# Kernel optimization log

Hardware: AMD Instinct MI355X
Metric: run time of the kernel (lower is better)

The kernel has to match this reference:

```python
import jax, jax.numpy as jnp
import numpy as np

DIM = 4096
BATCH = 8192
NUM_LAYERS = 6
STRENGTHS = (0.1, 0.1, 0.05)  # entail, contra, neutral
EPS_NORM = 1e-12  # torch F.normalize eps
MAX_NORM = 10.0


def _normalize(x, axis=-1):
    n = jnp.linalg.norm(x, axis=axis, keepdims=True)
    return x / jnp.maximum(n, EPS_NORM)


def setup_inputs() -> dict:
    key = jax.random.key(0)
    k0, k1, k2, k3 = jax.random.split(key, 4)
    return {
        "h0": jax.random.normal(k0, (BATCH, DIM), dtype=jnp.float32),
        "anchor_entail": jax.random.normal(k1, (DIM,), dtype=jnp.float32),
        "anchor_contra": jax.random.normal(k2, (DIM,), dtype=jnp.float32),
        "anchor_neutral": jax.random.normal(k3, (DIM,), dtype=jnp.float32),
    }


def reference(h0, anchor_entail, anchor_contra, anchor_neutral):
    # Normalized fixed anchor directions, stacked [3, dim] (E, C, N)
    dirs = jnp.stack([
        _normalize(anchor_entail, axis=0),
        _normalize(anchor_contra, axis=0),
        _normalize(anchor_neutral, axis=0),
    ])  # [3, dim]
    strengths = jnp.asarray(STRENGTHS, dtype=h0.dtype)  # [3]

    def step(h, _):
        h_n = _normalize(h)                         # [B, dim]
        align = jnp.einsum("bd,kd->bk", h_n, dirs)  # [B, 3]
        div = 1.0 - align                           # divergence_from_alignment
        tens = jnp.maximum(div, 0.0)                # tension (clamp min=0)
        # normalized direction away from each anchor: [B, 3, dim]
        vec = _normalize(h[:, None, :] - dirs[None, :, :])
        force = jnp.einsum("bk,bkd->bd", strengths[None, :] * div, vec)
        h = h - force
        h_norm = jnp.linalg.norm(h, axis=-1, keepdims=True)
        h = jnp.where(h_norm > MAX_NORM, h * (MAX_NORM / (h_norm + 1e-8)), h)
        return h, (align, div, tens)

    h_final, (aligns, divs, tensions) = jax.lax.scan(step, h0, None, length=NUM_LAYERS)
    # traces: [num_layers, B, 3] with anchor order (entail, contra, neutral)
    return h_final, aligns, divs, tensions
```

## Files before the change

kernel.cpp:

```cpp
#include <hip/hip_runtime.h>


constexpr int DIM = 4096;
constexpr int BATCH = 8192;
constexpr int NLAYERS = 6;
constexpr int TPB = 256;
constexpr int VPT = DIM / (TPB * 4);

constexpr size_t HOUT = (size_t)BATCH * DIM;
constexpr size_t TRACE = (size_t)NLAYERS * BATCH * 3;
constexpr size_t OFF_ALIGN = HOUT;
constexpr size_t OFF_DIV   = HOUT + TRACE;
constexpr size_t OFF_TENS  = HOUT + 2 * TRACE;

__device__ __forceinline__ float wave_red(float v) {
#pragma unroll
  for (int off = 32; off > 0; off >>= 1) v += __shfl_down(v, off, 64);
  return v;
}

__global__ __launch_bounds__(TPB) void gram_kernel(
    const float* __restrict__ an0, const float* __restrict__ an1,
    const float* __restrict__ an2, float* __restrict__ ws) {
  const int tid = threadIdx.x;
  float r[6];
#pragma unroll
  for (int i = 0; i < 6; ++i) r[i] = 0.f;
#pragma unroll
  for (int j = 0; j < VPT; ++j) {
    const int idx = (tid + j * TPB) * 4;
    const float4 x = *(const float4*)(an0 + idx);
    const float4 y = *(const float4*)(an1 + idx);
    const float4 z = *(const float4*)(an2 + idx);
    r[0] += x.x*x.x + x.y*x.y + x.z*x.z + x.w*x.w;
    r[1] += y.x*y.x + y.y*y.y + y.z*y.z + y.w*y.w;
    r[2] += z.x*z.x + z.y*z.y + z.z*z.z + z.w*z.w;
    r[3] += x.x*y.x + x.y*y.y + x.z*y.z + x.w*y.w;
    r[4] += x.x*z.x + x.y*z.y + x.z*z.z + x.w*z.w;
    r[5] += y.x*z.x + y.y*z.y + y.z*z.z + y.w*z.w;
  }
  __shared__ float lds[4][6];
  const int lane = tid & 63, wv = tid >> 6;
#pragma unroll
  for (int i = 0; i < 6; ++i) r[i] = wave_red(r[i]);
  if (lane == 0) {
#pragma unroll
    for (int i = 0; i < 6; ++i) lds[wv][i] = r[i];
  }
  __syncthreads();
  if (tid == 0) {
#pragma unroll
    for (int i = 0; i < 6; ++i)
      r[i] = lds[0][i] + lds[1][i] + lds[2][i] + lds[3][i];
    const float n0 = fmaxf(sqrtf(r[0]), 1e-12f);
    const float n1 = fmaxf(sqrtf(r[1]), 1e-12f);
    const float n2 = fmaxf(sqrtf(r[2]), 1e-12f);
    ws[0] = n0; ws[1] = n1; ws[2] = n2;
    ws[3] = r[3] / (n0 * n1);
    ws[4] = r[4] / (n0 * n2);
    ws[5] = r[5] / (n1 * n2);
    ws[6] = r[0] / (n0 * n0);
    ws[7] = r[1] / (n1 * n1);
    ws[8] = r[2] / (n2 * n2);
  }
}

__global__ __launch_bounds__(TPB) void collapse_kernel(
    const float* __restrict__ h0,
    const float* __restrict__ an0,
    const float* __restrict__ an1,
    const float* __restrict__ an2,
    const float* __restrict__ ws,
    float* __restrict__ out) {
  const int b = blockIdx.x;
  const int tid = threadIdx.x;
  const float* hrow = h0 + (size_t)b * DIM;

  float4 hv[VPT];
  float r[4] = {0.f, 0.f, 0.f, 0.f};
#pragma unroll
  for (int j = 0; j < VPT; ++j) {
    const int idx = (tid + j * TPB) * 4;
    hv[j] = *(const float4*)(hrow + idx);
    const float4 x = *(const float4*)(an0 + idx);
    const float4 y = *(const float4*)(an1 + idx);
    const float4 z = *(const float4*)(an2 + idx);
    const float4 h = hv[j];
    r[0] += h.x*h.x + h.y*h.y + h.z*h.z + h.w*h.w;
    r[1] += h.x*x.x + h.y*x.y + h.z*x.z + h.w*x.w;
    r[2] += h.x*y.x + h.y*y.y + h.z*y.z + h.w*y.w;
    r[3] += h.x*z.x + h.y*z.y + h.z*z.z + h.w*z.w;
  }

  __shared__ float lds[4][4];
  __shared__ float coef[4];
  const int lane = tid & 63, wv = tid >> 6;
#pragma unroll
  for (int i = 0; i < 4; ++i) r[i] = wave_red(r[i]);
  if (lane == 0) {
#pragma unroll
    for (int i = 0; i < 4; ++i) lds[wv][i] = r[i];
  }
  __syncthreads();

  if (tid == 0) {
#pragma unroll
    for (int i = 0; i < 4; ++i)
      r[i] = lds[0][i] + lds[1][i] + lds[2][i] + lds[3][i];
    const float n0 = ws[0], n1 = ws[1], n2 = ws[2];
    float G[3][3];
    G[0][1] = G[1][0] = ws[3];
    G[0][2] = G[2][0] = ws[4];
    G[1][2] = G[2][1] = ws[5];
    G[0][0] = ws[6]; G[1][1] = ws[7]; G[2][2] = ws[8];

    const float str[3] = {0.1f, 0.1f, 0.05f};
    float s = r[0];
    float d[3] = {r[1] / n0, r[2] / n1, r[3] / n2};
    float A = 1.f;
    float B[3] = {0.f, 0.f, 0.f};

#pragma unroll
    for (int l = 0; l < NLAYERS; ++l) {
      const float hn = fmaxf(sqrtf(s), 1e-12f);
      float al[3], dv[3], c[3];
#pragma unroll
      for (int k = 0; k < 3; ++k) {
        al[k] = d[k] / hn;
        dv[k] = 1.f - al[k];
        const float rr = fmaxf(sqrtf(s - 2.f * d[k] + G[k][k]), 1e-12f);
        c[k] = str[k] * dv[k] / rr;
      }
#pragma unroll
      for (int k = 0; k < 3; ++k) {
        const size_t o = (size_t)l * (BATCH * 3) + (size_t)b * 3 + k;
        out[OFF_ALIGN + o] = al[k];
        out[OFF_DIV + o]   = dv[k];
        out[OFF_TENS + o]  = fmaxf(dv[k], 0.f);
      }
      const float a = 1.f - (c[0] + c[1] + c[2]);
      float dn[3];
#pragma unroll
      for (int j = 0; j < 3; ++j)
        dn[j] = a * d[j] + c[0] * G[0][j] + c[1] * G[1][j] + c[2] * G[2][j];
      float sn = a * a * s + 2.f * a * (c[0]*d[0] + c[1]*d[1] + c[2]*d[2]);
#pragma unroll
      for (int k = 0; k < 3; ++k)
#pragma unroll
        for (int j = 0; j < 3; ++j) sn += c[k] * c[j] * G[k][j];
      A = a * A;
#pragma unroll
      for (int j = 0; j < 3; ++j) B[j] = a * B[j] + c[j];
      s = sn;
#pragma unroll
      for (int j = 0; j < 3; ++j) d[j] = dn[j];
      const float hn2 = sqrtf(s);
      if (hn2 > 10.0f) {
        const float sc = 10.0f / (hn2 + 1e-8f);
        A *= sc;
#pragma unroll
        for (int j = 0; j < 3; ++j) { B[j] *= sc; d[j] *= sc; }
        s *= sc * sc;
      }
    }
    coef[0] = A;
    coef[1] = B[0] / n0;
    coef[2] = B[1] / n1;
    coef[3] = B[2] / n2;
  }
  __syncthreads();
  const float A = coef[0], w0 = coef[1], w1 = coef[2], w2 = coef[3];

  float* orow = out + (size_t)b * DIM;
#pragma unroll
  for (int j = 0; j < VPT; ++j) {
    const int idx = (tid + j * TPB) * 4;
    const float4 x = *(const float4*)(an0 + idx);
    const float4 y = *(const float4*)(an1 + idx);
    const float4 z = *(const float4*)(an2 + idx);
    const float4 h = hv[j];
    float4 o;
    o.x = A * h.x + w0 * x.x + w1 * y.x + w2 * z.x;
    o.y = A * h.y + w0 * x.y + w1 * y.y + w2 * z.y;
    o.z = A * h.z + w0 * x.z + w1 * y.z + w2 * z.z;
    o.w = A * h.w + w0 * x.w + w1 * y.w + w2 * z.w;
    *(float4*)(orow + idx) = o;
  }
}

extern "C" void kernel_launch(void* const* d_in, const int* in_sizes, int n_in,
                              void* d_out, int out_size, void* d_ws, size_t ws_size,
                              hipStream_t stream) {
  const float* h0  = (const float*)d_in[0];
  const float* an0 = (const float*)d_in[1];
  const float* an1 = (const float*)d_in[2];
  const float* an2 = (const float*)d_in[3];
  float* out = (float*)d_out;
  float* ws  = (float*)d_ws;
  gram_kernel<<<1, TPB, 0, stream>>>(an0, an1, an2, ws);
  collapse_kernel<<<BATCH, TPB, 0, stream>>>(h0, an0, an1, an2, ws, out);
}
```

Before: 259.7 us.

## Assign one wavefront per row and use nontemporal output stores

Each row is now handled by a single 64-lane wavefront instead of a 256-thread block. Reductions become xor-shuffle all-reduces, and every lane redundantly runs the small 6-layer scalar recurrence, which removes LDS traffic and both block barriers. Divisions and square roots are replaced with hardware rcp/rsq approximations, and the output row is written with nontemporal stores. Each thread now holds 16 float4 of h in registers, which raises register pressure. The approximate rcp/rsq also shifts numerics slightly.

```diff
diff --git a/kernel.cpp b/kernel.cpp
--- a/kernel.cpp
+++ b/kernel.cpp
@@ -1,11 +1,15 @@
 #include <hip/hip_runtime.h>
 
+
+typedef float nf4 __attribute__((ext_vector_type(4)));
 
 constexpr int DIM = 4096;
 constexpr int BATCH = 8192;
 constexpr int NLAYERS = 6;
 constexpr int TPB = 256;
-constexpr int VPT = DIM / (TPB * 4);
+constexpr int WAVES = TPB / 64;
+constexpr int CPT = DIM / (64 * 4);
+constexpr int GVPT = DIM / (TPB * 4);
 
 constexpr size_t HOUT = (size_t)BATCH * DIM;
 constexpr size_t TRACE = (size_t)NLAYERS * BATCH * 3;
@@ -13,6 +17,12 @@
 constexpr size_t OFF_DIV   = HOUT + TRACE;
 constexpr size_t OFF_TENS  = HOUT + 2 * TRACE;
 
+__device__ __forceinline__ float wave_allred(float v) {
+#pragma unroll
+  for (int m = 1; m < 64; m <<= 1) v += __shfl_xor(v, m, 64);
+  return v;
+}
+
 __device__ __forceinline__ float wave_red(float v) {
 #pragma unroll
   for (int off = 32; off > 0; off >>= 1) v += __shfl_down(v, off, 64);
@@ -27,7 +37,7 @@
 #pragma unroll
   for (int i = 0; i < 6; ++i) r[i] = 0.f;
 #pragma unroll
-  for (int j = 0; j < VPT; ++j) {
+  for (int j = 0; j < GVPT; ++j) {
     const int idx = (tid + j * TPB) * 4;
     const float4 x = *(const float4*)(an0 + idx);
     const float4 y = *(const float4*)(an1 + idx);
@@ -65,72 +75,65 @@
   }
 }
 
-__global__ __launch_bounds__(TPB) void collapse_kernel(
+__global__ __launch_bounds__(TPB, 4) void collapse_kernel(
     const float* __restrict__ h0,
     const float* __restrict__ an0,
     const float* __restrict__ an1,
     const float* __restrict__ an2,
     const float* __restrict__ ws,
     float* __restrict__ out) {
-  const int b = blockIdx.x;
-  const int tid = threadIdx.x;
+  const int lane = threadIdx.x & 63;
+  const int wv = threadIdx.x >> 6;
+  const int b = blockIdx.x * WAVES + wv;
   const float* hrow = h0 + (size_t)b * DIM;
 
-  float4 hv[VPT];
-  float r[4] = {0.f, 0.f, 0.f, 0.f};
-#pragma unroll
-  for (int j = 0; j < VPT; ++j) {
-    const int idx = (tid + j * TPB) * 4;
+  float4 hv[CPT];
+  float r0 = 0.f, r1 = 0.f, r2 = 0.f, r3 = 0.f;
+#pragma unroll
+  for (int j = 0; j < CPT; ++j) {
+    const int idx = (lane + j * 64) * 4;
     hv[j] = *(const float4*)(hrow + idx);
     const float4 x = *(const float4*)(an0 + idx);
     const float4 y = *(const float4*)(an1 + idx);
     const float4 z = *(const float4*)(an2 + idx);
     const float4 h = hv[j];
-    r[0] += h.x*h.x + h.y*h.y + h.z*h.z + h.w*h.w;
-    r[1] += h.x*x.x + h.y*x.y + h.z*x.z + h.w*x.w;
-    r[2] += h.x*y.x + h.y*y.y + h.z*y.z + h.w*y.w;
-    r[3] += h.x*z.x + h.y*z.y + h.z*z.z + h.w*z.w;
-  }
-
-  __shared__ float lds[4][4];
-  __shared__ float coef[4];
-  const int lane = tid & 63, wv = tid >> 6;
-#pragma unroll
-  for (int i = 0; i < 4; ++i) r[i] = wave_red(r[i]);
-  if (lane == 0) {
-#pragma unroll
-    for (int i = 0; i < 4; ++i) lds[wv][i] = r[i];
-  }
-  __syncthreads();
-
-  if (tid == 0) {
-#pragma unroll
-    for (int i = 0; i < 4; ++i)
-      r[i] = lds[0][i] + lds[1][i] + lds[2][i] + lds[3][i];
-    const float n0 = ws[0], n1 = ws[1], n2 = ws[2];
-    float G[3][3];
-    G[0][1] = G[1][0] = ws[3];
-    G[0][2] = G[2][0] = ws[4];
-    G[1][2] = G[2][1] = ws[5];
-    G[0][0] = ws[6]; G[1][1] = ws[7]; G[2][2] = ws[8];
-
-    const float str[3] = {0.1f, 0.1f, 0.05f};
-    float s = r[0];
-    float d[3] = {r[1] / n0, r[2] / n1, r[3] / n2};
-    float A = 1.f;
-    float B[3] = {0.f, 0.f, 0.f};
-
-#pragma unroll
-    for (int l = 0; l < NLAYERS; ++l) {
-      const float hn = fmaxf(sqrtf(s), 1e-12f);
-      float al[3], dv[3], c[3];
-#pragma unroll
-      for (int k = 0; k < 3; ++k) {
-        al[k] = d[k] / hn;
-        dv[k] = 1.f - al[k];
-        const float rr = fmaxf(sqrtf(s - 2.f * d[k] + G[k][k]), 1e-12f);
-        c[k] = str[k] * dv[k] / rr;
-      }
+    r0 += h.x*h.x + h.y*h.y + h.z*h.z + h.w*h.w;
+    r1 += h.x*x.x + h.y*x.y + h.z*x.z + h.w*x.w;
+    r2 += h.x*y.x + h.y*y.y + h.z*y.z + h.w*y.w;
+    r3 += h.x*z.x + h.y*z.y + h.z*z.z + h.w*z.w;
+  }
+  r0 = wave_allred(r0);
+  r1 = wave_allred(r1);
+  r2 = wave_allred(r2);
+  r3 = wave_allred(r3);
+
+  const float n0 = ws[0], n1 = ws[1], n2 = ws[2];
+  float G[3][3];
+  G[0][1] = G[1][0] = ws[3];
+  G[0][2] = G[2][0] = ws[4];
+  G[1][2] = G[2][1] = ws[5];
+  G[0][0] = ws[6]; G[1][1] = ws[7]; G[2][2] = ws[8];
+
+  const float str[3] = {0.1f, 0.1f, 0.05f};
+  float s = r0;
+  float d[3] = {r1 * __builtin_amdgcn_rcpf(n0),
+                r2 * __builtin_amdgcn_rcpf(n1),
+                r3 * __builtin_amdgcn_rcpf(n2)};
+  float A = 1.f;
+  float B[3] = {0.f, 0.f, 0.f};
+
+#pragma unroll
+  for (int l = 0; l < NLAYERS; ++l) {
+    const float inv_hn = __builtin_amdgcn_rsqf(s);
+    float al[3], dv[3], c[3];
+#pragma unroll
+    for (int k = 0; k < 3; ++k) {
+      al[k] = d[k] * inv_hn;
+      dv[k] = 1.f - al[k];
+      const float rrsq = s - 2.f * d[k] + G[k][k];
+      c[k] = str[k] * dv[k] * __builtin_amdgcn_rsqf(fmaxf(rrsq, 1e-24f));
+    }
+    if (lane == 0) {
 #pragma unroll
       for (int k = 0; k < 3; ++k) {
         const size_t o = (size_t)l * (BATCH * 3) + (size_t)b * 3 + k;
@@ -138,53 +141,51 @@
         out[OFF_DIV + o]   = dv[k];
         out[OFF_TENS + o]  = fmaxf(dv[k], 0.f);
       }
-      const float a = 1.f - (c[0] + c[1] + c[2]);
-      float dn[3];
-#pragma unroll
-      for (int j = 0; j < 3; ++j)
-        dn[j] = a * d[j] + c[0] * G[0][j] + c[1] * G[1][j] + c[2] * G[2][j];
-      float sn = a * a * s + 2.f * a * (c[0]*d[0] + c[1]*d[1] + c[2]*d[2]);
-#pragma unroll
-      for (int k = 0; k < 3; ++k)
-#pragma unroll
-        for (int j = 0; j < 3; ++j) sn += c[k] * c[j] * G[k][j];
-      A = a * A;
-#pragma unroll
-      for (int j = 0; j < 3; ++j) B[j] = a * B[j] + c[j];
-      s = sn;
-#pragma unroll
-      for (int j = 0; j < 3; ++j) d[j] = dn[j];
-      const float hn2 = sqrtf(s);
-      if (hn2 > 10.0f) {
-        const float sc = 10.0f / (hn2 + 1e-8f);
-        A *= sc;
-#pragma unroll
-        for (int j = 0; j < 3; ++j) { B[j] *= sc; d[j] *= sc; }
-        s *= sc * sc;
-      }
     }
-    coef[0] = A;
-    coef[1] = B[0] / n0;
-    coef[2] = B[1] / n1;
-    coef[3] = B[2] / n2;
-  }
-  __syncthreads();
-  const float A = coef[0], w0 = coef[1], w1 = coef[2], w2 = coef[3];
+    const float a = 1.f - (c[0] + c[1] + c[2]);
+    float dn[3];
+#pragma unroll
+    for (int j = 0; j < 3; ++j)
+      dn[j] = a * d[j] + c[0] * G[0][j] + c[1] * G[1][j] + c[2] * G[2][j];
+    float sn = a * a * s + 2.f * a * (c[0]*d[0] + c[1]*d[1] + c[2]*d[2]);
+#pragma unroll
+    for (int k = 0; k < 3; ++k)
+#pragma unroll
+      for (int j = 0; j < 3; ++j) sn += c[k] * c[j] * G[k][j];
+    A = a * A;
+#pragma unroll
+    for (int j = 0; j < 3; ++j) B[j] = a * B[j] + c[j];
+    s = sn;
+#pragma unroll
+    for (int j = 0; j < 3; ++j) d[j] = dn[j];
+    if (s > 100.0f) {
+      const float hn2 = s * __builtin_amdgcn_rsqf(s);
+      const float sc = 10.0f * __builtin_amdgcn_rcpf(hn2 + 1e-8f);
+      A *= sc;
+#pragma unroll
+      for (int j = 0; j < 3; ++j) { B[j] *= sc; d[j] *= sc; }
+      s *= sc * sc;
+    }
+  }
+
+  const float w0 = B[0] * __builtin_amdgcn_rcpf(n0);
+  const float w1 = B[1] * __builtin_amdgcn_rcpf(n1);
+  const float w2 = B[2] * __builtin_amdgcn_rcpf(n2);
 
   float* orow = out + (size_t)b * DIM;
 #pragma unroll
-  for (int j = 0; j < VPT; ++j) {
-    const int idx = (tid + j * TPB) * 4;
+  for (int j = 0; j < CPT; ++j) {
+    const int idx = (lane + j * 64) * 4;
     const float4 x = *(const float4*)(an0 + idx);
     const float4 y = *(const float4*)(an1 + idx);
     const float4 z = *(const float4*)(an2 + idx);
     const float4 h = hv[j];
-    float4 o;
+    nf4 o;
     o.x = A * h.x + w0 * x.x + w1 * y.x + w2 * z.x;
     o.y = A * h.y + w0 * x.y + w1 * y.y + w2 * z.y;
     o.z = A * h.z + w0 * x.z + w1 * y.z + w2 * z.z;
     o.w = A * h.w + w0 * x.w + w1 * y.w + w2 * z.w;
-    *(float4*)(orow + idx) = o;
+    __builtin_nontemporal_store(o, (nf4*)(orow + idx));
   }
 }
 
@@ -198,5 +199,5 @@
   float* out = (float*)d_out;
   float* ws  = (float*)d_ws;
   gram_kernel<<<1, TPB, 0, stream>>>(an0, an1, an2, ws);
-  collapse_kernel<<<BATCH, TPB, 0, stream>>>(h0, an0, an1, an2, ws, out);
-}
+  collapse_kernel<<<BATCH / WAVES, TPB, 0, stream>>>(h0, an0, an1, an2, ws, out);
+}
```

After: 315.8 us. 1.22x slower.
